# Optimization experiments

Measured on AMD Instinct MI355X. Metric: run time of the kernel, lower is better.

Reference implementation:

```python
import jax, jax.numpy as jnp
import numpy as np

BS = 128  # block size for gating tiles


def setup_inputs() -> dict:
    key = jax.random.key(0)
    k1, k2, k3 = jax.random.split(key, 3)
    batch, dim_in, dim_out = 1536, 1536, 4608
    X = jax.random.normal(k1, (batch, dim_in), dtype=jnp.float32)
    W = jax.random.normal(k2, (dim_in, dim_out), dtype=jnp.float32)
    G = jax.random.normal(k3, (batch, dim_in // BS, dim_out // BS), dtype=jnp.float32)
    return {"X": X, "W": W, "G": G}


def reference(X, W, G):
    # Block-gated matmul: Y[b, j] = sum_i X[b, i] * W[i, j] * G[b, i//BS, j//BS]
    B, DI = X.shape
    DO = W.shape[1]
    NI, NJ = DI // BS, DO // BS
    Xr = X.reshape(B, NI, BS)               # [B, NI, bs]
    Wr = W.reshape(NI, BS, NJ, BS)          # [NI, bs, NJ, bs]
    # per-input-block partial products gated by G, summed over input blocks
    Y = jnp.einsum('bik,ikjl,bij->bjl', Xr, Wr, G)  # [B, NJ, bs]
    s = Y.sum()
    return s * s
```

## Files before the change

kernel.cpp:

```cpp
#include <hip/hip_runtime.h>


#define B_DIM 1536
#define DI    1536
#define DO    4608
#define NI    12
#define NJ    36
#define GROW  (NI * NJ)
#define BPW   8
#define K2_WAVES  (24 * (B_DIM / BPW))
#define K2_BLOCKS (K2_WAVES / 4)

__global__ __launch_bounds__(256) void wsum_kernel(const float* __restrict__ W,
                                                   float* __restrict__ WsumT) {
    int g    = blockIdx.x * 4 + (threadIdx.x >> 6);
    int lane = threadIdx.x & 63;
    int i = g / 18;
    int w = g - i * 18;
    const float4* p = (const float4*)(W + (size_t)i * DO + (size_t)w * 256);
    float4 v = p[lane];
    float s = (v.x + v.y) + (v.z + v.w);
    #pragma unroll
    for (int off = 16; off > 0; off >>= 1) s += __shfl_xor(s, off, 64);
    if (lane == 0)  WsumT[(size_t)(2 * w)     * DI + i] = s;
    if (lane == 32) WsumT[(size_t)(2 * w + 1) * DI + i] = s;
}

__global__ __launch_bounds__(256, 4) void gated_kernel(const float* __restrict__ X,
                                                       const float* __restrict__ G,
                                                       const float* __restrict__ WsumT,
                                                       float* __restrict__ partials) {
    __shared__ float4 gs4[BPW * 72 / 4];
    __shared__ float red[4];
    float* gs = (float*)gs4;

    const int t     = threadIdx.x;
    const int w     = t >> 6;
    const int lane  = t & 63;
    const int wave0 = blockIdx.x * 4;
    const int brng  = wave0 / 24;
    const int a     = (wave0 % 24) >> 2;
    const int b0    = brng * BPW;
    const int iblk  = (wave0 % 24) + w;
    const int i     = iblk * 64 + lane;
    const int d     = w >> 1;

    for (int e = t; e < BPW * 72; e += 256) {
        int b = e / 72, r = e - b * 72;
        gs[e] = G[(size_t)(b0 + b) * GROW + (size_t)(2 * a) * NJ + r];
    }

    float wv[NJ];
    #pragma unroll
    for (int k = 0; k < NJ; ++k) wv[k] = WsumT[(size_t)k * DI + i];
    #pragma unroll
    for (int k = 0; k < NJ; ++k) asm("" : "+v"(wv[k]));

    __syncthreads();

    const float* xp = X + (size_t)b0 * DI + i;
    float s = 0.f;
    #pragma unroll
    for (int bb = 0; bb < BPW; ++bb) {
        float x = xp[(size_t)bb * DI];
        const float4* gp = (const float4*)(gs + bb * 72 + d * 36);
        float d0 = 0.f, d1 = 0.f;
        #pragma unroll
        for (int k4 = 0; k4 < 9; ++k4) {
            float4 gv = gp[k4];
            d0 = fmaf(wv[4*k4+0], gv.x, d0);
            d1 = fmaf(wv[4*k4+1], gv.y, d1);
            d0 = fmaf(wv[4*k4+2], gv.z, d0);
            d1 = fmaf(wv[4*k4+3], gv.w, d1);
        }
        s = fmaf(x, d0 + d1, s);
    }

    #pragma unroll
    for (int off = 1; off < 64; off <<= 1) s += __shfl_xor(s, off, 64);
    if (lane == 0) red[w] = s;
    __syncthreads();
    if (t == 0)
        partials[blockIdx.x] = (red[0] + red[1]) + (red[2] + red[3]);
}

__global__ __launch_bounds__(256) void finish_kernel(const float* __restrict__ partials,
                                                     float* __restrict__ out) {
    __shared__ float red[4];
    const int t = threadIdx.x;
    float s = 0.f;
    for (int e = t; e < K2_BLOCKS; e += 256) s += partials[e];
    #pragma unroll
    for (int off = 1; off < 64; off <<= 1) s += __shfl_xor(s, off, 64);
    const int w = t >> 6, lane = t & 63;
    if (lane == 0) red[w] = s;
    __syncthreads();
    if (t == 0) {
        float tot = (red[0] + red[1]) + (red[2] + red[3]);
        out[0] = tot * tot;
    }
}

extern "C" void kernel_launch(void* const* d_in, const int* in_sizes, int n_in,
                              void* d_out, int out_size, void* d_ws, size_t ws_size,
                              hipStream_t stream) {
    const float* X = (const float*)d_in[0];
    const float* W = (const float*)d_in[1];
    const float* G = (const float*)d_in[2];
    float* out = (float*)d_out;

    float* WsumT    = (float*)d_ws;
    float* partials = WsumT + (size_t)NJ * DI;

    wsum_kernel<<<(DI * 18) / 4, 256, 0, stream>>>(W, WsumT);
    gated_kernel<<<K2_BLOCKS, 256, 0, stream>>>(X, G, WsumT, partials);
    finish_kernel<<<1, 256, 0, stream>>>(partials, out);
}
```

Baseline: 89.79 us.

## Fuse three kernels into one cooperative kernel with grid syncs

Merges the W column-sum, the gated reduction and the final reduction into a single cooperative launch of 768 blocks. Grid-wide barriers replace the kernel boundaries. Each block prefetches its G tile and X values before the first barrier, so those loads overlap the W pass, and BPW grows to 12 to fit the fixed grid. This removes two launch gaps and their tails, at the cost of two grid syncs and more registers held across the barrier.

```diff
diff --git a/kernel.cpp b/kernel.cpp
--- a/kernel.cpp
+++ b/kernel.cpp
@@ -1,4 +1,7 @@
 #include <hip/hip_runtime.h>
+#include <hip/hip_cooperative_groups.h>
+
+namespace cg = cooperative_groups;
 
 
 #define B_DIM 1536
@@ -7,73 +10,82 @@
 #define NI    12
 #define NJ    36
 #define GROW  (NI * NJ)
-#define BPW   8
-#define K2_WAVES  (24 * (B_DIM / BPW))
-#define K2_BLOCKS (K2_WAVES / 4)
+#define BPW   12
+#define NBLK  768
+#define P2_WAVES (NBLK * 4)
+#define P1_PER_WAVE 9
 
-__global__ __launch_bounds__(256) void wsum_kernel(const float* __restrict__ W,
-                                                   float* __restrict__ WsumT) {
-    int g    = blockIdx.x * 4 + (threadIdx.x >> 6);
-    int lane = threadIdx.x & 63;
-    int i = g / 18;
-    int w = g - i * 18;
-    const float4* p = (const float4*)(W + (size_t)i * DO + (size_t)w * 256);
-    float4 v = p[lane];
-    float s = (v.x + v.y) + (v.z + v.w);
+__global__ __launch_bounds__(256, 4) void fused_kernel(
+    const float* __restrict__ X, const float* __restrict__ W,
+    const float* __restrict__ G, float* __restrict__ WsumT,
+    float* __restrict__ partials, float* __restrict__ out)
+{
+    __shared__ float gs[BPW * 72];
+    __shared__ float red[4];
+
+    const int t    = threadIdx.x;
+    const int w    = t >> 6;
+    const int lane = t & 63;
+    const int beta = blockIdx.x;
+    const int wg   = beta * 4 + w;
+
+    float4 v[P1_PER_WAVE];
     #pragma unroll
-    for (int off = 16; off > 0; off >>= 1) s += __shfl_xor(s, off, 64);
-    if (lane == 0)  WsumT[(size_t)(2 * w)     * DI + i] = s;
-    if (lane == 32) WsumT[(size_t)(2 * w + 1) * DI + i] = s;
-}
+    for (int q = 0; q < P1_PER_WAVE; ++q) {
+        int g = wg + q * P2_WAVES;
+        int i1 = g / 18, p = g - i1 * 18;
+        v[q] = ((const float4*)(W + (size_t)i1 * DO + (size_t)p * 256))[lane];
+    }
+    #pragma unroll
+    for (int q = 0; q < P1_PER_WAVE; ++q) {
+        int g = wg + q * P2_WAVES;
+        int i1 = g / 18, p = g - i1 * 18;
+        float s1 = (v[q].x + v[q].y) + (v[q].z + v[q].w);
+        #pragma unroll
+        for (int off = 16; off > 0; off >>= 1) s1 += __shfl_xor(s1, off, 64);
+        if (lane == 0)  WsumT[(size_t)(2 * p)     * DI + i1] = s1;
+        if (lane == 32) WsumT[(size_t)(2 * p + 1) * DI + i1] = s1;
+    }
 
-__global__ __launch_bounds__(256, 4) void gated_kernel(const float* __restrict__ X,
-                                                       const float* __restrict__ G,
-                                                       const float* __restrict__ WsumT,
-                                                       float* __restrict__ partials) {
-    __shared__ float4 gs4[BPW * 72 / 4];
-    __shared__ float red[4];
-    float* gs = (float*)gs4;
-
-    const int t     = threadIdx.x;
-    const int w     = t >> 6;
-    const int lane  = t & 63;
-    const int wave0 = blockIdx.x * 4;
-    const int brng  = wave0 / 24;
-    const int a     = (wave0 % 24) >> 2;
-    const int b0    = brng * BPW;
-    const int iblk  = (wave0 % 24) + w;
-    const int i     = iblk * 64 + lane;
-    const int d     = w >> 1;
+    const int brng = beta / 6;
+    const int c    = beta - brng * 6;
+    const int b0   = brng * BPW;
+    const int iblk = 4 * c + w;
+    const int i    = iblk * 64 + lane;
+    const int d    = w >> 1;
 
     for (int e = t; e < BPW * 72; e += 256) {
         int b = e / 72, r = e - b * 72;
-        gs[e] = G[(size_t)(b0 + b) * GROW + (size_t)(2 * a) * NJ + r];
+        gs[e] = G[(size_t)(b0 + b) * GROW + (size_t)(2 * c) * NJ + r];
     }
+    const float* xp = X + (size_t)b0 * DI + i;
+    float xv[BPW];
+    #pragma unroll
+    for (int bb = 0; bb < BPW; ++bb) xv[bb] = xp[(size_t)bb * DI];
+    #pragma unroll
+    for (int bb = 0; bb < BPW; ++bb) asm("" : "+v"(xv[bb]));
+
+    __threadfence();
+    cg::this_grid().sync();
 
     float wv[NJ];
     #pragma unroll
     for (int k = 0; k < NJ; ++k) wv[k] = WsumT[(size_t)k * DI + i];
-    #pragma unroll
-    for (int k = 0; k < NJ; ++k) asm("" : "+v"(wv[k]));
 
-    __syncthreads();
-
-    const float* xp = X + (size_t)b0 * DI + i;
     float s = 0.f;
     #pragma unroll
     for (int bb = 0; bb < BPW; ++bb) {
-        float x = xp[(size_t)bb * DI];
         const float4* gp = (const float4*)(gs + bb * 72 + d * 36);
         float d0 = 0.f, d1 = 0.f;
         #pragma unroll
         for (int k4 = 0; k4 < 9; ++k4) {
             float4 gv = gp[k4];
-            d0 = fmaf(wv[4*k4+0], gv.x, d0);
-            d1 = fmaf(wv[4*k4+1], gv.y, d1);
-            d0 = fmaf(wv[4*k4+2], gv.z, d0);
-            d1 = fmaf(wv[4*k4+3], gv.w, d1);
+            d0 = fmaf(wv[4 * k4 + 0], gv.x, d0);
+            d1 = fmaf(wv[4 * k4 + 1], gv.y, d1);
+            d0 = fmaf(wv[4 * k4 + 2], gv.z, d0);
+            d1 = fmaf(wv[4 * k4 + 3], gv.w, d1);
         }
-        s = fmaf(x, d0 + d1, s);
+        s = fmaf(xv[bb], d0 + d1, s);
     }
 
     #pragma unroll
@@ -81,23 +93,23 @@
     if (lane == 0) red[w] = s;
     __syncthreads();
     if (t == 0)
-        partials[blockIdx.x] = (red[0] + red[1]) + (red[2] + red[3]);
-}
+        partials[beta] = (red[0] + red[1]) + (red[2] + red[3]);
 
-__global__ __launch_bounds__(256) void finish_kernel(const float* __restrict__ partials,
-                                                     float* __restrict__ out) {
-    __shared__ float red[4];
-    const int t = threadIdx.x;
-    float s = 0.f;
-    for (int e = t; e < K2_BLOCKS; e += 256) s += partials[e];
-    #pragma unroll
-    for (int off = 1; off < 64; off <<= 1) s += __shfl_xor(s, off, 64);
-    const int w = t >> 6, lane = t & 63;
-    if (lane == 0) red[w] = s;
-    __syncthreads();
-    if (t == 0) {
-        float tot = (red[0] + red[1]) + (red[2] + red[3]);
-        out[0] = tot * tot;
+    __threadfence();
+    cg::this_grid().sync();
+
+    if (beta == 0) {
+        float ss = 0.f;
+        #pragma unroll
+        for (int e = 0; e < 3; ++e) ss += partials[t + e * 256];
+        #pragma unroll
+        for (int off = 1; off < 64; off <<= 1) ss += __shfl_xor(ss, off, 64);
+        if (lane == 0) red[w] = ss;
+        __syncthreads();
+        if (t == 0) {
+            float tot = (red[0] + red[1]) + (red[2] + red[3]);
+            out[0] = tot * tot;
+        }
     }
 }
 
@@ -112,7 +124,8 @@
     float* WsumT    = (float*)d_ws;
     float* partials = WsumT + (size_t)NJ * DI;
 
-    wsum_kernel<<<(DI * 18) / 4, 256, 0, stream>>>(W, WsumT);
-    gated_kernel<<<K2_BLOCKS, 256, 0, stream>>>(X, G, WsumT, partials);
-    finish_kernel<<<1, 256, 0, stream>>>(partials, out);
+    void* args[] = { (void*)&X, (void*)&W, (void*)&G,
+                     (void*)&WsumT, (void*)&partials, (void*)&out };
+    hipLaunchCooperativeKernel((const void*)fused_kernel,
+                               dim3(NBLK), dim3(256), args, 0, stream);
 }
```

After: 342.0 us. +280.8%, slower.

## Reassociate gated sum: precompute H = X^T G per block, fuse with W row-sum

Applied to the files above, without the earlier changes.

Reorders the contraction so phase A computes H[j,i] = sum_b X[b,i]*G[b,ib,j] in 128-row batch chunks, staging the G slice in shared memory. The same launch also computes the W row-block sums on separate blocks. Phase B then reduces the 24 partial H slices and dots them with WsumT. This removes the per-batch-row reload of G tiles and WsumT registers, and overlaps the W read with the X*G work. In exchange it writes and reads a 24x36x1536 partial buffer and uses only 144 compute blocks, which may limit parallelism.

```diff
diff --git a/kernel.cpp b/kernel.cpp
--- a/kernel.cpp
+++ b/kernel.cpp
@@ -7,89 +7,105 @@
 #define NI    12
 #define NJ    36
 #define GROW  (NI * NJ)
-#define BPW   8
-#define K2_WAVES  (24 * (B_DIM / BPW))
-#define K2_BLOCKS (K2_WAVES / 4)
+#define HGRID (NJ * DI)
+#define NSP   (NI * 2)
+#define NHB   144
+#define WUPW  3
+#define NWW   (27648 / WUPW)
+#define NWB   (NWW / 4)
+#define NB_A  (NHB + NWB)
+#define NB_B  (HGRID / 256)
 
-__global__ __launch_bounds__(256) void wsum_kernel(const float* __restrict__ W,
-                                                   float* __restrict__ WsumT) {
-    int g    = blockIdx.x * 4 + (threadIdx.x >> 6);
-    int lane = threadIdx.x & 63;
-    int i = g / 18;
-    int w = g - i * 18;
-    const float4* p = (const float4*)(W + (size_t)i * DO + (size_t)w * 256);
-    float4 v = p[lane];
-    float s = (v.x + v.y) + (v.z + v.w);
-    #pragma unroll
-    for (int off = 16; off > 0; off >>= 1) s += __shfl_xor(s, off, 64);
-    if (lane == 0)  WsumT[(size_t)(2 * w)     * DI + i] = s;
-    if (lane == 32) WsumT[(size_t)(2 * w + 1) * DI + i] = s;
+__global__ __launch_bounds__(256) void phaseA(const float* __restrict__ X,
+                                              const float* __restrict__ W,
+                                              const float* __restrict__ G,
+                                              float* __restrict__ WsumT,
+                                              float* __restrict__ Hp) {
+    __shared__ float gsl[128 * NJ];
+    const int t    = threadIdx.x;
+    const int w    = t >> 6;
+    const int lane = t & 63;
+    const int beta = blockIdx.x;
+
+    if (beta < NHB) {
+        const int ib = beta / NI;
+        const int bc = beta - ib * NI;
+        const int b0 = bc * 128;
+        for (int e = t; e < 128 * NJ; e += 256) {
+            int b = e / NJ, r = e - b * NJ;
+            gsl[e] = G[(size_t)(b0 + b) * GROW + ib * NJ + r];
+        }
+        __syncthreads();
+
+        const int il = t & 127;
+        const int bp = t >> 7;
+        const float* xp = X + (size_t)(b0 + bp) * DI + ib * 128 + il;
+        float acc[NJ];
+        #pragma unroll
+        for (int k = 0; k < NJ; ++k) acc[k] = 0.f;
+
+        #pragma unroll 4
+        for (int bl = 0; bl < 64; ++bl) {
+            float x = xp[(size_t)bl * 2 * DI];
+            const float4* g4 = (const float4*)(gsl + (2 * bl + bp) * NJ);
+            #pragma unroll
+            for (int k = 0; k < 9; ++k) {
+                float4 g = g4[k];
+                acc[4 * k + 0] = fmaf(x, g.x, acc[4 * k + 0]);
+                acc[4 * k + 1] = fmaf(x, g.y, acc[4 * k + 1]);
+                acc[4 * k + 2] = fmaf(x, g.z, acc[4 * k + 2]);
+                acc[4 * k + 3] = fmaf(x, g.w, acc[4 * k + 3]);
+            }
+        }
+        float* hp = Hp + (size_t)(bc * 2 + bp) * HGRID + ib * 128 + il;
+        #pragma unroll
+        for (int k = 0; k < NJ; ++k) hp[(size_t)k * DI] = acc[k];
+    } else {
+        const int wgW = (beta - NHB) * 4 + w;
+        float4 v[WUPW];
+        int ii[WUPW], pp[WUPW];
+        #pragma unroll
+        for (int q = 0; q < WUPW; ++q) {
+            int g = wgW + q * NWW;
+            ii[q] = g / 18;
+            pp[q] = g - ii[q] * 18;
+            v[q] = ((const float4*)(W + (size_t)ii[q] * DO + pp[q] * 256))[lane];
+        }
+        #pragma unroll
+        for (int q = 0; q < WUPW; ++q) {
+            float s1 = (v[q].x + v[q].y) + (v[q].z + v[q].w);
+            #pragma unroll
+            for (int off = 16; off > 0; off >>= 1) s1 += __shfl_xor(s1, off, 64);
+            if (lane == 0)  WsumT[(size_t)(2 * pp[q])     * DI + ii[q]] = s1;
+            if (lane == 32) WsumT[(size_t)(2 * pp[q] + 1) * DI + ii[q]] = s1;
+        }
+    }
 }
 
-__global__ __launch_bounds__(256, 4) void gated_kernel(const float* __restrict__ X,
-                                                       const float* __restrict__ G,
-                                                       const float* __restrict__ WsumT,
-                                                       float* __restrict__ partials) {
-    __shared__ float4 gs4[BPW * 72 / 4];
+__global__ __launch_bounds__(256) void phaseB(const float* __restrict__ WsumT,
+                                              const float* __restrict__ Hp,
+                                              float* __restrict__ partials) {
     __shared__ float red[4];
-    float* gs = (float*)gs4;
-
-    const int t     = threadIdx.x;
-    const int w     = t >> 6;
-    const int lane  = t & 63;
-    const int wave0 = blockIdx.x * 4;
-    const int brng  = wave0 / 24;
-    const int a     = (wave0 % 24) >> 2;
-    const int b0    = brng * BPW;
-    const int iblk  = (wave0 % 24) + w;
-    const int i     = iblk * 64 + lane;
-    const int d     = w >> 1;
-
-    for (int e = t; e < BPW * 72; e += 256) {
-        int b = e / 72, r = e - b * 72;
-        gs[e] = G[(size_t)(b0 + b) * GROW + (size_t)(2 * a) * NJ + r];
-    }
-
-    float wv[NJ];
+    const int t = threadIdx.x;
+    const size_t T = (size_t)blockIdx.x * 256 + t;
+    float h = 0.f;
     #pragma unroll
-    for (int k = 0; k < NJ; ++k) wv[k] = WsumT[(size_t)k * DI + i];
-    #pragma unroll
-    for (int k = 0; k < NJ; ++k) asm("" : "+v"(wv[k]));
-
-    __syncthreads();
-
-    const float* xp = X + (size_t)b0 * DI + i;
-    float s = 0.f;
-    #pragma unroll
-    for (int bb = 0; bb < BPW; ++bb) {
-        float x = xp[(size_t)bb * DI];
-        const float4* gp = (const float4*)(gs + bb * 72 + d * 36);
-        float d0 = 0.f, d1 = 0.f;
-        #pragma unroll
-        for (int k4 = 0; k4 < 9; ++k4) {
-            float4 gv = gp[k4];
-            d0 = fmaf(wv[4*k4+0], gv.x, d0);
-            d1 = fmaf(wv[4*k4+1], gv.y, d1);
-            d0 = fmaf(wv[4*k4+2], gv.z, d0);
-            d1 = fmaf(wv[4*k4+3], gv.w, d1);
-        }
-        s = fmaf(x, d0 + d1, s);
-    }
-
+    for (int sp = 0; sp < NSP; ++sp) h += Hp[(size_t)sp * HGRID + T];
+    float s = WsumT[T] * h;
     #pragma unroll
     for (int off = 1; off < 64; off <<= 1) s += __shfl_xor(s, off, 64);
+    const int w = t >> 6, lane = t & 63;
     if (lane == 0) red[w] = s;
     __syncthreads();
     if (t == 0)
         partials[blockIdx.x] = (red[0] + red[1]) + (red[2] + red[3]);
 }
 
-__global__ __launch_bounds__(256) void finish_kernel(const float* __restrict__ partials,
-                                                     float* __restrict__ out) {
+__global__ __launch_bounds__(256) void phaseC(const float* __restrict__ partials,
+                                              float* __restrict__ out) {
     __shared__ float red[4];
     const int t = threadIdx.x;
-    float s = 0.f;
-    for (int e = t; e < K2_BLOCKS; e += 256) s += partials[e];
+    float s = (t < NB_B) ? partials[t] : 0.f;
     #pragma unroll
     for (int off = 1; off < 64; off <<= 1) s += __shfl_xor(s, off, 64);
     const int w = t >> 6, lane = t & 63;
@@ -110,9 +126,10 @@
     float* out = (float*)d_out;
 
     float* WsumT    = (float*)d_ws;
-    float* partials = WsumT + (size_t)NJ * DI;
+    float* Hp       = WsumT + HGRID;
+    float* partials = Hp + (size_t)NSP * HGRID;
 
-    wsum_kernel<<<(DI * 18) / 4, 256, 0, stream>>>(W, WsumT);
-    gated_kernel<<<K2_BLOCKS, 256, 0, stream>>>(X, G, WsumT, partials);
-    finish_kernel<<<1, 256, 0, stream>>>(partials, out);
+    phaseA<<<NB_A, 256, 0, stream>>>(X, W, G, WsumT, Hp);
+    phaseB<<<NB_B, 256, 0, stream>>>(WsumT, Hp, partials);
+    phaseC<<<1, 256, 0, stream>>>(partials, out);
 }
```

Result: slower. 94.55 us (+5.3%).
